# Kernel optimization log

Measured on AMD Instinct MI355X. Metric: run time of the kernel, lower is better.

## Reference

```python
import jax, jax.numpy as jnp
import numpy as np

N_HEAD = 8
LN_EPS = 1e-5


def layernorm(x, g, b):
    m = x.mean(-1, keepdims=True)
    var = x.var(-1, keepdims=True)
    return (x - m) / jnp.sqrt(var + LN_EPS) * g + b


def mha(xq, xkv, key_pad, w, b, wo, bo):
    # w: [3, D, D] (q,k,v proj), key_pad: [B, Nk] bool, True = ignore
    B, Nq, D = xq.shape
    H, dh = N_HEAD, D // N_HEAD
    q = (xq @ w[0] + b[0]).reshape(B, Nq, H, dh)
    k = (xkv @ w[1] + b[1]).reshape(B, -1, H, dh)
    v = (xkv @ w[2] + b[2]).reshape(B, -1, H, dh)
    s = jnp.einsum('bqhd,bkhd->bhqk', q, k) * (1.0 / np.float32(np.sqrt(dh)))
    s = jnp.where(key_pad[:, None, None, :], jnp.float32(-1e9), s)
    a = jax.nn.softmax(s, axis=-1)
    o = jnp.einsum('bhqk,bkhd->bqhd', a, v).reshape(B, Nq, D)
    return o @ wo + bo


def coattn_layer(v, q, v_pad, q_pad, aw, ab, awo, abo, lg, lb, fw1, fb1, fw2, fb2):
    # self-attention + residual + LN
    v_a = layernorm(v + mha(v, v, v_pad, aw[0], ab[0], awo[0], abo[0]), lg[0], lb[0])
    q_a = layernorm(q + mha(q, q, q_pad, aw[1], ab[1], awo[1], abo[1]), lg[1], lb[1])
    # cross attention: note qv_attn consumes OUTPUT of vq_attn (as in original)
    vq_out = mha(v_a, q_a, q_pad, aw[2], ab[2], awo[2], abo[2])
    qv_out = mha(q_a, vq_out, v_pad, aw[3], ab[3], awo[3], abo[3])
    v = layernorm(v + vq_out, lg[2], lb[2])
    q = layernorm(q + qv_out, lg[3], lb[3])
    # FFN (fc -> relu -> fc), residual + LN
    v = layernorm(v + (jax.nn.relu(v @ fw1[0] + fb1[0]) @ fw2[0] + fb2[0]), lg[4], lb[4])
    q = layernorm(q + (jax.nn.relu(q @ fw1[1] + fb1[1]) @ fw2[1] + fb2[1]), lg[5], lb[5])
    return v, q


def setup_inputs() -> dict:
    key = jax.random.key(0)
    B, NV, NQ, D, L = 8, 512, 512, 512, 4
    DF = 4 * D
    ks = jax.random.split(key, 12)
    sd = 0.02
    inp = {}
    inp['v'] = jax.random.normal(ks[0], (B, NV, D), jnp.float32)
    inp['q'] = jax.random.normal(ks[1], (B, NQ, D), jnp.float32)
    vm = jax.random.randint(ks[2], (B, NV), 0, 2, jnp.int32)
    qm = jax.random.randint(ks[3], (B, NQ), 0, 2, jnp.int32)
    inp['v_mask'] = vm.at[:, 0].set(1)  # ensure >=1 valid token per row
    inp['q_mask'] = qm.at[:, 0].set(1)
    inp['attn_w'] = sd * jax.random.normal(ks[4], (L, 4, 3, D, D), jnp.float32)
    inp['attn_b'] = jnp.zeros((L, 4, 3, D), jnp.float32)
    inp['attn_wo'] = sd * jax.random.normal(ks[5], (L, 4, D, D), jnp.float32)
    inp['attn_bo'] = jnp.zeros((L, 4, D), jnp.float32)
    inp['ln_g'] = jnp.ones((L, 6, D), jnp.float32)
    inp['ln_b'] = jnp.zeros((L, 6, D), jnp.float32)
    inp['ffn_w1'] = sd * jax.random.normal(ks[6], (L, 2, D, DF), jnp.float32)
    inp['ffn_b1'] = jnp.zeros((L, 2, DF), jnp.float32)
    inp['ffn_w2'] = sd * jax.random.normal(ks[7], (L, 2, DF, D), jnp.float32)
    inp['ffn_b2'] = jnp.zeros((L, 2, D), jnp.float32)
    inp['att_w'] = sd * jax.random.normal(ks[8], (D,), jnp.float32)
    inp['att_b'] = jnp.zeros((), jnp.float32)
    return inp


def reference(v, q, attn_w, attn_b, attn_wo, attn_bo, ln_g, ln_b,
              ffn_w1, ffn_b1, ffn_w2, ffn_b2, att_w, att_b, v_mask, q_mask):
    v_pad = v_mask == 0  # True = pad (original: ~v_mask.bool())
    q_pad = q_mask == 0
    L = attn_w.shape[0]
    for i in range(L):
        v, q = coattn_layer(v, q, v_pad, q_pad,
                            attn_w[i], attn_b[i], attn_wo[i], attn_bo[i],
                            ln_g[i], ln_b[i],
                            ffn_w1[i], ffn_b1[i], ffn_w2[i], ffn_b2[i])
    # att_net(v_i * q_j) is a bilinear form: sum_k v_bvk * q_bqk * w_k + bias
    s = jnp.einsum('bvk,bqk,k->bvq', v, q, att_w) + att_b
    cross_mask = v_pad[:, :, None] | q_pad[:, None, :]
    s = jnp.where(cross_mask, jnp.float32(-1e9), s)
    att_maps = jax.nn.softmax(s, axis=-1)
    v_num, q_num = v.shape[1], q.shape[1]
    seq_scale = 1.0 / np.float32(np.sqrt(v_num * q_num))
    return jnp.einsum('bvk,bvq,bqk->bk', v, att_maps, q) * seq_scale
```

## Files before the change

kernel.cpp:

```cpp
#include <hip/hip_runtime.h>
#include <hip/hip_bf16.h>

typedef __hip_bfloat16 bf16;
typedef __attribute__((ext_vector_type(8))) short short8;
typedef __attribute__((ext_vector_type(4))) short short4v;
typedef __attribute__((ext_vector_type(4))) float f32x4;

#define AS1 __attribute__((address_space(1)))
#define AS3 __attribute__((address_space(3)))

#define B_  8
#define N_  512
#define D_  512
#define H_  8
#define DH_ 64
#define DF_ 2048
#define L_  4

static __device__ __forceinline__ short bfbits(float x) {
  bf16 t = __float2bfloat16(x);
  return *reinterpret_cast<short*>(&t);
}

__global__ __launch_bounds__(256) void k_prep(const float* __restrict__ in,
                                              float* __restrict__ f,
                                              bf16* __restrict__ b, int n) {
  int i = blockIdx.x * 256 + threadIdx.x;
  if (i < n) { float v = in[i]; f[i] = v; b[i] = __float2bfloat16(v); }
}

__global__ __launch_bounds__(256) void k_wt(const float* __restrict__ aw_l,
                                            const float* __restrict__ awo_l,
                                            const float* __restrict__ fw1_l,
                                            const float* __restrict__ fw2_l,
                                            bf16* __restrict__ WT)
{
  __shared__ float Ls[32][33];
  int bx = blockIdx.x;
  const float* src; bf16* dst; int R, C, tr, tc;
  if (bx < 4096) {
    int id = bx >> 8, t = bx & 255;
    int m = id >> 2, part = id & 3;
    src = (part < 3) ? (aw_l + ((long)m * 3 + part) * D_ * D_)
                     : (awo_l + (long)m * D_ * D_);
    dst = WT + (long)id * 262144; R = 512; C = 512; tr = t >> 4; tc = t & 15;
  } else if (bx < 6144) {
    int q = bx - 4096; int id = q >> 10; int t = q & 1023;
    src = fw1_l + (long)id * D_ * DF_; dst = WT + 4194304 + (long)id * 1048576;
    R = 512; C = 2048; tr = t >> 6; tc = t & 63;
  } else {
    int q = bx - 6144; int id = q >> 10; int t = q & 1023;
    src = fw2_l + (long)id * DF_ * D_; dst = WT + 6291456 + (long)id * 1048576;
    R = 2048; C = 512; tr = t >> 4; tc = t & 15;
  }
  int tt = threadIdx.x;
#pragma unroll
  for (int p = 0; p < 4; ++p) {
    int idx = tt + p * 256; int lr = idx >> 5, lc = idx & 31;
    Ls[lr][lc] = src[(long)(tr * 32 + lr) * C + tc * 32 + lc];
  }
  __syncthreads();
#pragma unroll
  for (int p = 0; p < 4; ++p) {
    int idx = tt + p * 256; int lr = idx >> 5, lc = idx & 31;
    dst[(long)(tc * 32 + lr) * R + tr * 32 + lc] = __float2bfloat16(Ls[lc][lr]);
  }
}

template<int BN>
__global__ __launch_bounds__(256, 2) void k_mfma(
    const bf16* __restrict__ A, const bf16* __restrict__ A2,
    long aS, long aB, long aH, int lda,
    const bf16* __restrict__ Bm, long bS, long bB, long bH, int ldb,
    const float* __restrict__ bias, long biasS, float scale, int relu,
    float* __restrict__ Cf, long cfS, long cfB, long cfH, int ldcf,
    bf16* __restrict__ Cb, long cbS, long cbB, long cbH, int ldcb,
    int K, int Hh, int zPerS, int mode)
{
  constexpr int MI = (BN == 128) ? 4 : 2;
  constexpr int NI = 4;
  __shared__ short As[128 * 32];
  __shared__ short Bs[BN * 32];
  int tid = threadIdx.x;
  int w = tid >> 6, lane = tid & 63;
  int z = blockIdx.z;
  int s = z / zPerS; int zz = z - s * zPerS;
  int zb = zz / Hh, zh = zz - zb * Hh;
  int row0 = blockIdx.y * 128;
  int col0 = blockIdx.x * BN;
  const bf16* Asel = (mode == 1 && col0 >= 512) ? A2 : A;
  const bf16* Ab = Asel + s * aS + zb * aB + zh * aH;
  const bf16* Bb = Bm + s * bS + zb * bB + zh * bH;
  int rw = (BN == 128) ? ((w >> 1) * 64) : (w * 32);
  int cw = (BN == 128) ? ((w & 1) * 64) : 0;
  int quad = lane >> 4, l16 = lane & 15;

  f32x4 acc[MI][NI];
#pragma unroll
  for (int i = 0; i < MI; ++i)
#pragma unroll
    for (int j = 0; j < NI; ++j) acc[i][j] = {0.f, 0.f, 0.f, 0.f};

  for (int k0 = 0; k0 < K; k0 += 32) {
#pragma unroll
    for (int i = 0; i < 2; ++i) {
      int o = i * 4096 + w * 1024 + lane * 16;
      int r = o >> 6;
      const bf16* g = Ab + (long)(row0 + r) * lda + k0 + ((o & 63) >> 1);
      char* lp = (char*)As + i * 4096 + w * 1024;
      __builtin_amdgcn_global_load_lds((const AS1 void*)g, (AS3 void*)lp, 16, 0, 0);
    }
    constexpr int BI = (BN == 128) ? 2 : 1;
#pragma unroll
    for (int i = 0; i < BI; ++i) {
      int o = i * 4096 + w * 1024 + lane * 16;
      int r = o >> 6;
      const bf16* g = Bb + (long)(col0 + r) * ldb + k0 + ((o & 63) >> 1);
      char* lp = (char*)Bs + i * 4096 + w * 1024;
      __builtin_amdgcn_global_load_lds((const AS1 void*)g, (AS3 void*)lp, 16, 0, 0);
    }
    __syncthreads();
    short8 af[MI], bfr[NI];
#pragma unroll
    for (int mi = 0; mi < MI; ++mi)
      af[mi] = *(const short8*)&As[(rw + mi * 16 + l16) * 32 + quad * 8];
#pragma unroll
    for (int ni = 0; ni < NI; ++ni)
      bfr[ni] = *(const short8*)&Bs[(cw + ni * 16 + l16) * 32 + quad * 8];
#pragma unroll
    for (int mi = 0; mi < MI; ++mi)
#pragma unroll
      for (int ni = 0; ni < NI; ++ni)
        acc[mi][ni] = __builtin_amdgcn_mfma_f32_16x16x32_bf16(af[mi], bfr[ni], acc[mi][ni], 0, 0, 0);
    __syncthreads();
  }

  const float* bp = bias ? bias + s * biasS : nullptr;
#pragma unroll
  for (int mi = 0; mi < MI; ++mi)
#pragma unroll
    for (int ni = 0; ni < NI; ++ni) {
      int cg = col0 + cw + ni * 16 + l16;
      float bv = bp ? bp[cg] : 0.0f;
#pragma unroll
      for (int r = 0; r < 4; ++r) {
        int rg = row0 + rw + mi * 16 + quad * 4 + r;
        float v = acc[mi][ni][r] * scale + bv;
        if (relu) v = fmaxf(v, 0.0f);
        if (mode == 1) {
          bf16* base = Cb + s * cbS;
          if (cg < 512) base[(long)rg * 512 + cg] = __float2bfloat16(v);
          else if (cg < 1024) base[2097152 + (long)rg * 512 + (cg - 512)] = __float2bfloat16(v);
          else {
            int c2 = cg - 1024;
            base[4194304 + ((long)((rg >> 9) * 8 + (c2 >> 6)) * 64 + (c2 & 63)) * 512 + (rg & 511)]
                = __float2bfloat16(v);
          }
        } else {
          if (Cf) Cf[s * cfS + zb * cfB + zh * cfH + (long)rg * ldcf + cg] = v;
          if (Cb) Cb[s * cbS + zb * cbB + zh * cbH + (long)rg * ldcb + cg] = __float2bfloat16(v);
        }
      }
    }
}

__global__ __launch_bounds__(256, 2) void k_flash(
    const bf16* __restrict__ QKV, long sStride,
    const int* __restrict__ km0, const int* __restrict__ km1, float scale)
{
  __shared__ short Ks[2 * 128 * 32];
  __shared__ short Vs[4 * 64 * 32];
  __shared__ short Ps[4 * 64 * 32];
  int tid = threadIdx.x, w = tid >> 6, lane = tid & 63;
  int quad = lane >> 4, l16 = lane & 15;
  int s = blockIdx.z;
  const bf16* base = QKV + s * sStride;
  int bh = blockIdx.y, b = bh >> 3, h = bh & 7;
  int qt = blockIdx.x;
  const int* km = (s ? km1 : km0) + (b << 9);
  const bf16* Kg = base + 2097152;
  const bf16* Vt = base + 4194304;
  bf16* Og = (bf16*)base;

  int qrow = (b << 9) + (qt << 6) + (w << 4) + l16;
  short8 qf[2];
  qf[0] = *(const short8*)&base[(long)qrow * 512 + h * 64 + quad * 8];
  qf[1] = *(const short8*)&base[(long)qrow * 512 + h * 64 + 32 + quad * 8];

  float m_[4], l_[4];
  f32x4 acc_o[4];
#pragma unroll
  for (int r = 0; r < 4; ++r) { m_[r] = -3e38f; l_[r] = 0.f; }
#pragma unroll
  for (int ni = 0; ni < 4; ++ni) acc_o[ni] = {0.f, 0.f, 0.f, 0.f};

  for (int kt = 0; kt < 4; ++kt) {
    __syncthreads();
#pragma unroll
    for (int i = 0; i < 4; ++i) {
      int o = i * 4096 + w * 1024 + lane * 16;
      int kc = o >> 13, rem = o & 8191;
      int n = rem >> 6, cb = rem & 63;
      const bf16* g = Kg + ((long)((b << 9) + kt * 128 + n) << 9) + h * 64 + kc * 32 + (cb >> 1);
      char* lp = (char*)Ks + i * 4096 + w * 1024;
      __builtin_amdgcn_global_load_lds((const AS1 void*)g, (AS3 void*)lp, 16, 0, 0);
    }
#pragma unroll
    for (int i = 0; i < 4; ++i) {
      int o = i * 4096 + w * 1024 + lane * 16;
      int kc = o >> 12, rem = o & 4095;
      int d = rem >> 6, cb = rem & 63;
      const bf16* g = Vt + ((long)((bh << 6) + d) << 9) + kt * 128 + kc * 32 + (cb >> 1);
      char* lp = (char*)Vs + i * 4096 + w * 1024;
      __builtin_amdgcn_global_load_lds((const AS1 void*)g, (AS3 void*)lp, 16, 0, 0);
    }
    __syncthreads();
    f32x4 sa[8];
#pragma unroll
    for (int ni = 0; ni < 8; ++ni) sa[ni] = {0.f, 0.f, 0.f, 0.f};
#pragma unroll
    for (int kc = 0; kc < 2; ++kc)
#pragma unroll
      for (int ni = 0; ni < 8; ++ni) {
        short8 bfrag = *(const short8*)&Ks[kc * 4096 + (ni * 16 + l16) * 32 + quad * 8];
        sa[ni] = __builtin_amdgcn_mfma_f32_16x16x32_bf16(qf[kc], bfrag, sa[ni], 0, 0, 0);
      }
    float sv[8][4];
#pragma unroll
    for (int ni = 0; ni < 8; ++ni) {
      int kmv = km[kt * 128 + ni * 16 + l16];
#pragma unroll
      for (int r = 0; r < 4; ++r)
        sv[ni][r] = kmv ? sa[ni][r] * scale : -1e9f;
    }
#pragma unroll
    for (int r = 0; r < 4; ++r) {
      float rmax = sv[0][r];
#pragma unroll
      for (int ni = 1; ni < 8; ++ni) rmax = fmaxf(rmax, sv[ni][r]);
#pragma unroll
      for (int o = 1; o < 16; o <<= 1) rmax = fmaxf(rmax, __shfl_xor(rmax, o, 64));
      float newm = fmaxf(m_[r], rmax);
      float alpha = __expf(m_[r] - newm);
      float psum = 0.f;
#pragma unroll
      for (int ni = 0; ni < 8; ++ni) {
        float p = __expf(sv[ni][r] - newm);
        sv[ni][r] = p; psum += p;
      }
#pragma unroll
      for (int o = 1; o < 16; o <<= 1) psum += __shfl_xor(psum, o, 64);
      l_[r] = l_[r] * alpha + psum;
      m_[r] = newm;
#pragma unroll
      for (int ni = 0; ni < 4; ++ni) acc_o[ni][r] *= alpha;
    }
#pragma unroll
    for (int ni = 0; ni < 8; ++ni) {
      int j = ni * 16 + l16;
      short* pp = &Ps[(j >> 5) * 2048 + (w * 16 + quad * 4) * 32 + (j & 31)];
#pragma unroll
      for (int r = 0; r < 4; ++r) pp[r * 32] = bfbits(sv[ni][r]);
    }
    __syncthreads();
#pragma unroll
    for (int kcp = 0; kcp < 4; ++kcp) {
      short8 af = *(const short8*)&Ps[kcp * 2048 + (w * 16 + l16) * 32 + quad * 8];
#pragma unroll
      for (int ni = 0; ni < 4; ++ni) {
        short8 bfrag = *(const short8*)&Vs[kcp * 2048 + (ni * 16 + l16) * 32 + quad * 8];
        acc_o[ni] = __builtin_amdgcn_mfma_f32_16x16x32_bf16(af, bfrag, acc_o[ni], 0, 0, 0);
      }
    }
  }
  float linv[4];
#pragma unroll
  for (int r = 0; r < 4; ++r) linv[r] = 1.0f / l_[r];
#pragma unroll
  for (int ni = 0; ni < 4; ++ni)
#pragma unroll
    for (int r = 0; r < 4; ++r) {
      long row = (b << 9) + (qt << 6) + (w << 4) + quad * 4 + r;
      Og[row * 512 + h * 64 + ni * 16 + l16] = __float2bfloat16(acc_o[ni][r] * linv[r]);
    }
}

__global__ __launch_bounds__(256) void k_ln2(
    const float* x0, const float* r0, const float* g0, const float* b0,
    float* yf0, bf16* yb0,
    const float* x1, const float* r1, const float* g1, const float* b1,
    float* yf1, bf16* yb1)
{
  int sel = blockIdx.x >> 12;
  long row = blockIdx.x & 4095;
  const float* x = sel ? x1 : x0;
  const float* r = sel ? r1 : r0;
  const float* g = sel ? g1 : g0;
  const float* bb = sel ? b1 : b0;
  float* yf = sel ? yf1 : yf0;
  bf16* yb = sel ? yb1 : yb0;
  int t = threadIdx.x;
  const float* xr = x + row * D_;
  const float* rr = r + row * D_;
  float v0 = xr[t] + rr[t];
  float v1 = xr[t + 256] + rr[t + 256];
  float s = v0 + v1;
  float ss = v0 * v0 + v1 * v1;
#pragma unroll
  for (int o = 32; o > 0; o >>= 1) {
    s += __shfl_down(s, o, 64);
    ss += __shfl_down(ss, o, 64);
  }
  __shared__ float rs[4];
  __shared__ float rss[4];
  int lane = t & 63, wid = t >> 6;
  if (lane == 0) { rs[wid] = s; rss[wid] = ss; }
  __syncthreads();
  s = rs[0] + rs[1] + rs[2] + rs[3];
  ss = rss[0] + rss[1] + rss[2] + rss[3];
  float mean = s * (1.0f / D_);
  float var = ss * (1.0f / D_) - mean * mean;
  float rstd = rsqrtf(var + 1e-5f);
  float o0 = (v0 - mean) * rstd * g[t]       + bb[t];
  float o1 = (v1 - mean) * rstd * g[t + 256] + bb[t + 256];
  if (yf) { float* yr = yf + row * D_; yr[t] = o0; yr[t + 256] = o1; }
  if (yb) { bf16* yr = yb + row * D_; yr[t] = __float2bfloat16(o0); yr[t + 256] = __float2bfloat16(o1); }
}

__global__ __launch_bounds__(256) void k_softmax_x(float* __restrict__ S,
                                                   const int* __restrict__ vm,
                                                   const int* __restrict__ qm)
{
  int wrow = blockIdx.x * 4 + (threadIdx.x >> 6);
  int lane = threadIdx.x & 63;
  int b = wrow >> 9, i = wrow & 511;
  bool rowpad = (vm[(b << 9) + i] == 0);
  float* p = S + (long)wrow * 512;
  const int* qb = qm + (b << 9);
  int j0 = lane * 8;
  float4 a0 = *(const float4*)(p + j0);
  float4 a1 = *(const float4*)(p + j0 + 4);
  int4 m0 = *(const int4*)(qb + j0);
  int4 m1 = *(const int4*)(qb + j0 + 4);
  float v[8];
  v[0] = (rowpad || !m0.x) ? -1e9f : a0.x; v[1] = (rowpad || !m0.y) ? -1e9f : a0.y;
  v[2] = (rowpad || !m0.z) ? -1e9f : a0.z; v[3] = (rowpad || !m0.w) ? -1e9f : a0.w;
  v[4] = (rowpad || !m1.x) ? -1e9f : a1.x; v[5] = (rowpad || !m1.y) ? -1e9f : a1.y;
  v[6] = (rowpad || !m1.z) ? -1e9f : a1.z; v[7] = (rowpad || !m1.w) ? -1e9f : a1.w;
  float mx = v[0];
#pragma unroll
  for (int u = 1; u < 8; ++u) mx = fmaxf(mx, v[u]);
#pragma unroll
  for (int o = 1; o < 64; o <<= 1) mx = fmaxf(mx, __shfl_xor(mx, o, 64));
  float e[8], sum = 0.f;
#pragma unroll
  for (int u = 0; u < 8; ++u) { e[u] = __expf(v[u] - mx); sum += e[u]; }
#pragma unroll
  for (int o = 1; o < 64; o <<= 1) sum += __shfl_xor(sum, o, 64);
  float inv = 1.0f / sum;
  bf16 ob[8];
#pragma unroll
  for (int u = 0; u < 8; ++u) ob[u] = __float2bfloat16(e[u] * inv);
  bf16* pb = (bf16*)p;
  *(short8*)&pb[j0] = *(const short8*)ob;
}

__global__ __launch_bounds__(256) void k_vwqt(const float* __restrict__ V,
                                              const float* __restrict__ Q,
                                              const float* __restrict__ w,
                                              bf16* __restrict__ Vw, bf16* __restrict__ Qt)
{
  __shared__ float Ls[32][33];
  int bx = blockIdx.x, t = threadIdx.x;
  if (bx < 2048) {
    int i = bx * 1024 + t * 4;
    float4 v = *(const float4*)(V + i);
    int k = i & 511;
    bf16 o[4] = { __float2bfloat16(v.x * w[k]),     __float2bfloat16(v.y * w[k + 1]),
                  __float2bfloat16(v.z * w[k + 2]), __float2bfloat16(v.w * w[k + 3]) };
    *(short4v*)&Vw[i] = *(const short4v*)o;
  } else {
    int q = bx - 2048; int b = q >> 8; int tq = q & 255;
    int tr = tq >> 4, tc = tq & 15;
    const float* Qb = Q + (long)b * 262144;
    bf16* Qtb = Qt + (long)b * 262144;
#pragma unroll
    for (int p = 0; p < 4; ++p) {
      int idx = t + p * 256; int lr = idx >> 5, lc = idx & 31;
      Ls[lr][lc] = Qb[(long)(tr * 32 + lr) * 512 + tc * 32 + lc];
    }
    __syncthreads();
#pragma unroll
    for (int p = 0; p < 4; ++p) {
      int idx = t + p * 256; int lr = idx >> 5, lc = idx & 31;
      Qtb[(long)(tc * 32 + lr) * 512 + tr * 32 + lc] = __float2bfloat16(Ls[lc][lr]);
    }
  }
}

__global__ __launch_bounds__(256) void k_final_out(
    const float* __restrict__ V, const float* __restrict__ QT, float* __restrict__ out)
{
  int b = blockIdx.x >> 1;
  int k = ((blockIdx.x & 1) << 8) + threadIdx.x;
  const float* Vb = V + (long)b * N_ * D_ + k;
  const float* Tb = QT + (long)b * N_ * D_ + k;
  float acc = 0.0f;
  for (int i = 0; i < N_; ++i) acc += Vb[(long)i * D_] * Tb[(long)i * D_];
  out[b * D_ + k] = acc * (1.0f / 512.0f);
}

extern "C" void kernel_launch(void* const* d_in, const int* in_sizes, int n_in,
                              void* d_out, int out_size, void* d_ws, size_t ws_size,
                              hipStream_t stream)
{
  const float* in_v   = (const float*)d_in[0];
  const float* in_q   = (const float*)d_in[1];
  const int*   v_mask = (const int*)  d_in[2];
  const int*   q_mask = (const int*)  d_in[3];
  const float* aw  = (const float*)d_in[4];
  const float* ab  = (const float*)d_in[5];
  const float* awo = (const float*)d_in[6];
  const float* abo = (const float*)d_in[7];
  const float* lg  = (const float*)d_in[8];
  const float* lb  = (const float*)d_in[9];
  const float* fw1 = (const float*)d_in[10];
  const float* fb1 = (const float*)d_in[11];
  const float* fw2 = (const float*)d_in[12];
  const float* fb2 = (const float*)d_in[13];
  const float* atw = (const float*)d_in[14];
  const float* atb = (const float*)d_in[15];
  float* out = (float*)d_out;
  (void)atb;

  const int SZ = B_ * N_ * D_;
  char* wsb = (char*)d_ws;
  const long MB = 1024L * 1024;
  float* Vcur   = (float*)(wsb + 0 * MB);
  float* Qcur   = (float*)(wsb + 8 * MB);
  float* T      = (float*)(wsb + 16 * MB);
  bf16*  WT     = (bf16*) (wsb + 24 * MB);
  bf16*  Vcur_b = (bf16*) (wsb + 40 * MB);
  bf16*  Qcur_b = (bf16*) (wsb + 44 * MB);
  bf16*  VA_b   = (bf16*) (wsb + 48 * MB);
  bf16*  QA_b   = (bf16*) (wsb + 52 * MB);
  bf16*  VQ_b   = (bf16*) (wsb + 56 * MB);
  bf16*  QKV0   = (bf16*) (wsb + 60 * MB);
  bf16*  Hid    = (bf16*) (wsb + 84 * MB);
  float* T2     = (float*)(wsb + 116 * MB);
  float* Sf     = (float*)(wsb + 124 * MB);
  bf16*  Vw_b   = (bf16*) (wsb + 132 * MB);
  bf16*  Qt_b   = (bf16*) (wsb + 136 * MB);

  const long ZBIG = 1000000;
  const long TSTR = (long)(T2 - T);

  k_prep<<<8192, 256, 0, stream>>>(in_v, Vcur, Vcur_b, SZ);
  k_prep<<<8192, 256, 0, stream>>>(in_q, Qcur, Qcur_b, SZ);

  for (int l = 0; l < L_; ++l) {
    const float* lgl = lg + (long)l * 6 * D_;
    const float* lbl = lb + (long)l * 6 * D_;
    k_wt<<<8192, 256, 0, stream>>>(aw + (long)l * 12 * 262144,
                                   awo + (long)l * 4 * 262144,
                                   fw1 + (long)l * 2 * 1048576,
                                   fw2 + (long)l * 2 * 1048576, WT);
    k_mfma<128><<<dim3(12, 32, 2), 256, 0, stream>>>(
        Vcur_b, Vcur_b, 2097152, 0, 0, 512,
        WT, 1048576, 0, 0, 512,
        ab + (long)l * 4 * 1536, 1536, 1.f, 0,
        nullptr, 0, 0, 0, 0, QKV0, 6291456, 0, 0, 0,
        512, 1, 1, 1);
    k_flash<<<dim3(8, 64, 2), 256, 0, stream>>>(QKV0, 6291456, v_mask, q_mask, 0.125f);
    k_mfma<128><<<dim3(4, 32, 2), 256, 0, stream>>>(
        QKV0, QKV0, 6291456, 0, 0, 512,
        WT + 3 * 262144, 1048576, 0, 0, 512,
        abo + (long)l * 4 * 512, 512, 1.f, 0,
        T, TSTR, 0, 0, 512, nullptr, 0, 0, 0, 0,
        512, 1, 1, 0);
    k_ln2<<<8192, 256, 0, stream>>>(Vcur, T,  lgl + 0 * D_, lbl + 0 * D_, nullptr, VA_b,
                                    Qcur, T2, lgl + 1 * D_, lbl + 1 * D_, nullptr, QA_b);
    k_mfma<128><<<dim3(12, 32, 1), 256, 0, stream>>>(
        VA_b, QA_b, 0, 0, 0, 512,
        WT + 2 * 1048576, 0, 0, 0, 512,
        ab + (long)(l * 4 + 2) * 1536, 0, 1.f, 0,
        nullptr, 0, 0, 0, 0, QKV0, 0, 0, 0, 0,
        512, 1, 1, 1);
    k_flash<<<dim3(8, 64, 1), 256, 0, stream>>>(QKV0, 0, q_mask, q_mask, 0.125f);
    k_mfma<128><<<dim3(4, 32, 1), 256, 0, stream>>>(
        QKV0, QKV0, 0, 0, 0, 512,
        WT + (2 * 4 + 3) * 262144, 0, 0, 0, 512,
        abo + (long)(l * 4 + 2) * 512, 0, 1.f, 0,
        T, 0, 0, 0, 512, VQ_b, 0, 0, 0, 512,
        512, 1, 1, 0);
    k_mfma<128><<<dim3(12, 32, 1), 256, 0, stream>>>(
        QA_b, VQ_b, 0, 0, 0, 512,
        WT + 3 * 1048576, 0, 0, 0, 512,
        ab + (long)(l * 4 + 3) * 1536, 0, 1.f, 0,
        nullptr, 0, 0, 0, 0, QKV0, 0, 0, 0, 0,
        512, 1, 1, 1);
    k_flash<<<dim3(8, 64, 1), 256, 0, stream>>>(QKV0, 0, v_mask, v_mask, 0.125f);
    k_mfma<128><<<dim3(4, 32, 1), 256, 0, stream>>>(
        QKV0, QKV0, 0, 0, 0, 512,
        WT + (3 * 4 + 3) * 262144, 0, 0, 0, 512,
        abo + (long)(l * 4 + 3) * 512, 0, 1.f, 0,
        T2, 0, 0, 0, 512, nullptr, 0, 0, 0, 0,
        512, 1, 1, 0);
    k_ln2<<<8192, 256, 0, stream>>>(Vcur, T,  lgl + 2 * D_, lbl + 2 * D_, Vcur, Vcur_b,
                                    Qcur, T2, lgl + 3 * D_, lbl + 3 * D_, Qcur, Qcur_b);
    k_mfma<128><<<dim3(16, 32, 2), 256, 0, stream>>>(
        Vcur_b, Vcur_b, 2097152, 0, 0, 512,
        WT + 4194304, 1048576, 0, 0, 512,
        fb1 + (long)l * 2 * 2048, 2048, 1.f, 1,
        nullptr, 0, 0, 0, 0, Hid, 8388608, 0, 0, 2048,
        512, 1, 1, 0);
    k_mfma<128><<<dim3(4, 32, 2), 256, 0, stream>>>(
        Hid, Hid, 8388608, 0, 0, 2048,
        WT + 6291456, 1048576, 0, 0, 2048,
        fb2 + (long)l * 2 * 512, 512, 1.f, 0,
        T, TSTR, 0, 0, 512, nullptr, 0, 0, 0, 0,
        2048, 1, 1, 0);
    k_ln2<<<8192, 256, 0, stream>>>(Vcur, T,  lgl + 4 * D_, lbl + 4 * D_, Vcur, Vcur_b,
                                    Qcur, T2, lgl + 5 * D_, lbl + 5 * D_, Qcur, Qcur_b);
  }

  k_vwqt<<<4096, 256, 0, stream>>>(Vcur, Qcur, atw, Vw_b, Qt_b);
  k_mfma<128><<<dim3(4, 4, 8), 256, 0, stream>>>(
      Vw_b, Vw_b, 0, 262144, 0, 512, Qcur_b, 0, 262144, 0, 512,
      nullptr, 0, 1.f, 0,
      Sf, 0, 262144, 0, 512, nullptr, 0, 0, 0, 0,
      512, 1, ZBIG, 0);
  k_softmax_x<<<1024, 256, 0, stream>>>(Sf, v_mask, q_mask);
  k_mfma<128><<<dim3(4, 4, 8), 256, 0, stream>>>(
      (const bf16*)Sf, (const bf16*)Sf, 0, 524288, 0, 1024, Qt_b, 0, 262144, 0, 512,
      nullptr, 0, 1.f, 0,
      T, 0, 262144, 0, 512, nullptr, 0, 0, 0, 0,
      512, 1, ZBIG, 0);
  k_final_out<<<16, 256, 0, stream>>>(Vcur, T, out);

  (void)in_sizes; (void)n_in; (void)out_size; (void)ws_size;
}
```

Baseline: 1.571 ms.

## Split-K the N=512 output projections and fuse partial-sum reduction into LayerNorm

The output-projection and FFN-down GEMMs (N=512, only 128-256 blocks) now split K into two halves via an extra grid z dimension, each writing fp32 partials to separate buffers. The LayerNorm kernel sums both partials with the residual, replacing the old single-result add. The cross-attention projections also switch to the 64-wide tile, and a small kernel sums partials into bf16 for VQ. The aim is more blocks to fill the GPU, at the cost of extra fp32 partial traffic and one more launch.

```diff
diff --git a/kernel.cpp b/kernel.cpp
--- a/kernel.cpp
+++ b/kernel.cpp
@@ -75,7 +75,7 @@
     const float* __restrict__ bias, long biasS, float scale, int relu,
     float* __restrict__ Cf, long cfS, long cfB, long cfH, int ldcf,
     bf16* __restrict__ Cb, long cbS, long cbB, long cbH, int ldcb,
-    int K, int Hh, int zPerS, int mode)
+    int kLen, int Hh, int zPerS, int mode, int kSplit, long pStride)
 {
   constexpr int MI = (BN == 128) ? 4 : 2;
   constexpr int NI = 4;
@@ -84,13 +84,15 @@
   int tid = threadIdx.x;
   int w = tid >> 6, lane = tid & 63;
   int z = blockIdx.z;
+  int kk = 0;
+  if (kSplit > 1) { kk = z % kSplit; z /= kSplit; }
   int s = z / zPerS; int zz = z - s * zPerS;
   int zb = zz / Hh, zh = zz - zb * Hh;
   int row0 = blockIdx.y * 128;
   int col0 = blockIdx.x * BN;
   const bf16* Asel = (mode == 1 && col0 >= 512) ? A2 : A;
-  const bf16* Ab = Asel + s * aS + zb * aB + zh * aH;
-  const bf16* Bb = Bm + s * bS + zb * bB + zh * bH;
+  const bf16* Ab = Asel + s * aS + zb * aB + zh * aH + (long)kk * kLen;
+  const bf16* Bb = Bm + s * bS + zb * bB + zh * bH + (long)kk * kLen;
   int rw = (BN == 128) ? ((w >> 1) * 64) : (w * 32);
   int cw = (BN == 128) ? ((w & 1) * 64) : 0;
   int quad = lane >> 4, l16 = lane & 15;
@@ -101,7 +103,7 @@
 #pragma unroll
     for (int j = 0; j < NI; ++j) acc[i][j] = {0.f, 0.f, 0.f, 0.f};
 
-  for (int k0 = 0; k0 < K; k0 += 32) {
+  for (int k0 = 0; k0 < kLen; k0 += 32) {
 #pragma unroll
     for (int i = 0; i < 2; ++i) {
       int o = i * 4096 + w * 1024 + lane * 16;
@@ -135,7 +137,7 @@
     __syncthreads();
   }
 
-  const float* bp = bias ? bias + s * biasS : nullptr;
+  const float* bp = (bias && kk == 0) ? bias + s * biasS : nullptr;
 #pragma unroll
   for (int mi = 0; mi < MI; ++mi)
 #pragma unroll
@@ -157,7 +159,7 @@
                 = __float2bfloat16(v);
           }
         } else {
-          if (Cf) Cf[s * cfS + zb * cfB + zh * cfH + (long)rg * ldcf + cg] = v;
+          if (Cf) Cf[s * cfS + (long)kk * pStride + zb * cfB + zh * cfH + (long)rg * ldcf + cg] = v;
           if (Cb) Cb[s * cbS + zb * cbB + zh * cbH + (long)rg * ldcb + cg] = __float2bfloat16(v);
         }
       }
@@ -286,24 +288,23 @@
 }
 
 __global__ __launch_bounds__(256) void k_ln2(
-    const float* x0, const float* r0, const float* g0, const float* b0,
-    float* yf0, bf16* yb0,
-    const float* x1, const float* r1, const float* g1, const float* b1,
-    float* yf1, bf16* yb1)
+    const float* x0, const float* g0, const float* b0, float* yf0, bf16* yb0,
+    const float* x1, const float* g1, const float* b1, float* yf1, bf16* yb1,
+    const float* __restrict__ P, long pstr)
 {
   int sel = blockIdx.x >> 12;
   long row = blockIdx.x & 4095;
   const float* x = sel ? x1 : x0;
-  const float* r = sel ? r1 : r0;
   const float* g = sel ? g1 : g0;
   const float* bb = sel ? b1 : b0;
   float* yf = sel ? yf1 : yf0;
   bf16* yb = sel ? yb1 : yb0;
   int t = threadIdx.x;
   const float* xr = x + row * D_;
-  const float* rr = r + row * D_;
-  float v0 = xr[t] + rr[t];
-  float v1 = xr[t + 256] + rr[t + 256];
+  const float* ra = P + (sel ? 2 : 0) * pstr + row * D_;
+  const float* rb = ra + pstr;
+  float v0 = xr[t] + ra[t] + rb[t];
+  float v1 = xr[t + 256] + ra[t + 256] + rb[t + 256];
   float s = v0 + v1;
   float ss = v0 * v0 + v1 * v1;
 #pragma unroll
@@ -325,6 +326,18 @@
   float o1 = (v1 - mean) * rstd * g[t + 256] + bb[t + 256];
   if (yf) { float* yr = yf + row * D_; yr[t] = o0; yr[t + 256] = o1; }
   if (yb) { bf16* yr = yb + row * D_; yr[t] = __float2bfloat16(o0); yr[t + 256] = __float2bfloat16(o1); }
+}
+
+__global__ __launch_bounds__(256) void k_sum2bf(const float* __restrict__ a,
+                                                const float* __restrict__ b,
+                                                bf16* __restrict__ o)
+{
+  int i = (blockIdx.x * 256 + threadIdx.x) * 4;
+  float4 va = *(const float4*)(a + i);
+  float4 vb = *(const float4*)(b + i);
+  bf16 ov[4] = { __float2bfloat16(va.x + vb.x), __float2bfloat16(va.y + vb.y),
+                 __float2bfloat16(va.z + vb.z), __float2bfloat16(va.w + vb.w) };
+  *(short4v*)&o[i] = *(const short4v*)ov;
 }
 
 __global__ __launch_bounds__(256) void k_softmax_x(float* __restrict__ S,
@@ -438,22 +451,22 @@
   const long MB = 1024L * 1024;
   float* Vcur   = (float*)(wsb + 0 * MB);
   float* Qcur   = (float*)(wsb + 8 * MB);
-  float* T      = (float*)(wsb + 16 * MB);
-  bf16*  WT     = (bf16*) (wsb + 24 * MB);
-  bf16*  Vcur_b = (bf16*) (wsb + 40 * MB);
-  bf16*  Qcur_b = (bf16*) (wsb + 44 * MB);
-  bf16*  VA_b   = (bf16*) (wsb + 48 * MB);
-  bf16*  QA_b   = (bf16*) (wsb + 52 * MB);
-  bf16*  VQ_b   = (bf16*) (wsb + 56 * MB);
-  bf16*  QKV0   = (bf16*) (wsb + 60 * MB);
-  bf16*  Hid    = (bf16*) (wsb + 84 * MB);
-  float* T2     = (float*)(wsb + 116 * MB);
-  float* Sf     = (float*)(wsb + 124 * MB);
-  bf16*  Vw_b   = (bf16*) (wsb + 132 * MB);
-  bf16*  Qt_b   = (bf16*) (wsb + 136 * MB);
+  float* P0     = (float*)(wsb + 16 * MB);
+  const long PSZ = 2097152;
+  bf16*  WT     = (bf16*) (wsb + 48 * MB);
+  bf16*  Vcur_b = (bf16*) (wsb + 64 * MB);
+  bf16*  Qcur_b = (bf16*) (wsb + 68 * MB);
+  bf16*  VA_b   = (bf16*) (wsb + 72 * MB);
+  bf16*  QA_b   = (bf16*) (wsb + 76 * MB);
+  bf16*  VQ_b   = (bf16*) (wsb + 80 * MB);
+  bf16*  QKV0   = (bf16*) (wsb + 84 * MB);
+  bf16*  Hid    = (bf16*) (wsb + 108 * MB);
+  float* Sf     = P0;
+  bf16*  Vw_b   = (bf16*) (wsb + 24 * MB);
+  bf16*  Qt_b   = (bf16*) (wsb + 28 * MB);
+  float* Tfin   = (float*)(wsb + 32 * MB);
 
   const long ZBIG = 1000000;
-  const long TSTR = (long)(T2 - T);
 
   k_prep<<<8192, 256, 0, stream>>>(in_v, Vcur, Vcur_b, SZ);
   k_prep<<<8192, 256, 0, stream>>>(in_q, Qcur, Qcur_b, SZ);
@@ -470,58 +483,62 @@
         WT, 1048576, 0, 0, 512,
         ab + (long)l * 4 * 1536, 1536, 1.f, 0,
         nullptr, 0, 0, 0, 0, QKV0, 6291456, 0, 0, 0,
-        512, 1, 1, 1);
+        512, 1, 1, 1, 1, 0);
     k_flash<<<dim3(8, 64, 2), 256, 0, stream>>>(QKV0, 6291456, v_mask, q_mask, 0.125f);
-    k_mfma<128><<<dim3(4, 32, 2), 256, 0, stream>>>(
+    k_mfma<128><<<dim3(4, 32, 4), 256, 0, stream>>>(
         QKV0, QKV0, 6291456, 0, 0, 512,
         WT + 3 * 262144, 1048576, 0, 0, 512,
         abo + (long)l * 4 * 512, 512, 1.f, 0,
-        T, TSTR, 0, 0, 512, nullptr, 0, 0, 0, 0,
-        512, 1, 1, 0);
-    k_ln2<<<8192, 256, 0, stream>>>(Vcur, T,  lgl + 0 * D_, lbl + 0 * D_, nullptr, VA_b,
-                                    Qcur, T2, lgl + 1 * D_, lbl + 1 * D_, nullptr, QA_b);
+        P0, 2 * PSZ, 0, 0, 512, nullptr, 0, 0, 0, 0,
+        256, 1, 1, 0, 2, PSZ);
+    k_ln2<<<8192, 256, 0, stream>>>(Vcur, lgl + 0 * D_, lbl + 0 * D_, nullptr, VA_b,
+                                    Qcur, lgl + 1 * D_, lbl + 1 * D_, nullptr, QA_b,
+                                    P0, PSZ);
     k_mfma<128><<<dim3(12, 32, 1), 256, 0, stream>>>(
         VA_b, QA_b, 0, 0, 0, 512,
         WT + 2 * 1048576, 0, 0, 0, 512,
         ab + (long)(l * 4 + 2) * 1536, 0, 1.f, 0,
         nullptr, 0, 0, 0, 0, QKV0, 0, 0, 0, 0,
-        512, 1, 1, 1);
+        512, 1, 1, 1, 1, 0);
     k_flash<<<dim3(8, 64, 1), 256, 0, stream>>>(QKV0, 0, q_mask, q_mask, 0.125f);
-    k_mfma<128><<<dim3(4, 32, 1), 256, 0, stream>>>(
+    k_mfma<64><<<dim3(8, 32, 2), 256, 0, stream>>>(
         QKV0, QKV0, 0, 0, 0, 512,
         WT + (2 * 4 + 3) * 262144, 0, 0, 0, 512,
         abo + (long)(l * 4 + 2) * 512, 0, 1.f, 0,
-        T, 0, 0, 0, 512, VQ_b, 0, 0, 0, 512,
-        512, 1, 1, 0);
+        P0, 0, 0, 0, 512, nullptr, 0, 0, 0, 0,
+        256, 1, 1, 0, 2, PSZ);
+    k_sum2bf<<<2048, 256, 0, stream>>>(P0, P0 + PSZ, VQ_b);
     k_mfma<128><<<dim3(12, 32, 1), 256, 0, stream>>>(
         QA_b, VQ_b, 0, 0, 0, 512,
         WT + 3 * 1048576, 0, 0, 0, 512,
         ab + (long)(l * 4 + 3) * 1536, 0, 1.f, 0,
         nullptr, 0, 0, 0, 0, QKV0, 0, 0, 0, 0,
-        512, 1, 1, 1);
+        512, 1, 1, 1, 1, 0);
     k_flash<<<dim3(8, 64, 1), 256, 0, stream>>>(QKV0, 0, v_mask, v_mask, 0.125f);
-    k_mfma<128><<<dim3(4, 32, 1), 256, 0, stream>>>(
+    k_mfma<64><<<dim3(8, 32, 2), 256, 0, stream>>>(
         QKV0, QKV0, 0, 0, 0, 512,
         WT + (3 * 4 + 3) * 262144, 0, 0, 0, 512,
         abo + (long)(l * 4 + 3) * 512, 0, 1.f, 0,
-        T2, 0, 0, 0, 512, nullptr, 0, 0, 0, 0,
-        512, 1, 1, 0);
-    k_ln2<<<8192, 256, 0, stream>>>(Vcur, T,  lgl + 2 * D_, lbl + 2 * D_, Vcur, Vcur_b,
-                                    Qcur, T2, lgl + 3 * D_, lbl + 3 * D_, Qcur, Qcur_b);
+        P0 + 2 * PSZ, 0, 0, 0, 512, nullptr, 0, 0, 0, 0,
+        256, 1, 1, 0, 2, PSZ);
+    k_ln2<<<8192, 256, 0, stream>>>(Vcur, lgl + 2 * D_, lbl + 2 * D_, Vcur, Vcur_b,
+                                    Qcur, lgl + 3 * D_, lbl + 3 * D_, Qcur, Qcur_b,
+                                    P0, PSZ);
     k_mfma<128><<<dim3(16, 32, 2), 256, 0, stream>>>(
         Vcur_b, Vcur_b, 2097152, 0, 0, 512,
         WT + 4194304, 1048576, 0, 0, 512,
         fb1 + (long)l * 2 * 2048, 2048, 1.f, 1,
         nullptr, 0, 0, 0, 0, Hid, 8388608, 0, 0, 2048,
-        512, 1, 1, 0);
-    k_mfma<128><<<dim3(4, 32, 2), 256, 0, stream>>>(
+        512, 1, 1, 0, 1, 0);
+    k_mfma<128><<<dim3(4, 32, 4), 256, 0, stream>>>(
         Hid, Hid, 8388608, 0, 0, 2048,
         WT + 6291456, 1048576, 0, 0, 2048,
         fb2 + (long)l * 2 * 512, 512, 1.f, 0,
-        T, TSTR, 0, 0, 512, nullptr, 0, 0, 0, 0,
-        2048, 1, 1, 0);
-    k_ln2<<<8192, 256, 0, stream>>>(Vcur, T,  lgl + 4 * D_, lbl + 4 * D_, Vcur, Vcur_b,
-                                    Qcur, T2, lgl + 5 * D_, lbl + 5 * D_, Qcur, Qcur_b);
+        P0, 2 * PSZ, 0, 0, 512, nullptr, 0, 0, 0, 0,
+        1024, 1, 1, 0, 2, PSZ);
+    k_ln2<<<8192, 256, 0, stream>>>(Vcur, lgl + 4 * D_, lbl + 4 * D_, Vcur, Vcur_b,
+                                    Qcur, lgl + 5 * D_, lbl + 5 * D_, Qcur, Qcur_b,
+                                    P0, PSZ);
   }
 
   k_vwqt<<<4096, 256, 0, stream>>>(Vcur, Qcur, atw, Vw_b, Qt_b);
@@ -529,14 +546,14 @@
       Vw_b, Vw_b, 0, 262144, 0, 512, Qcur_b, 0, 262144, 0, 512,
       nullptr, 0, 1.f, 0,
       Sf, 0, 262144, 0, 512, nullptr, 0, 0, 0, 0,
-      512, 1, ZBIG, 0);
+      512, 1, ZBIG, 0, 1, 0);
   k_softmax_x<<<1024, 256, 0, stream>>>(Sf, v_mask, q_mask);
   k_mfma<128><<<dim3(4, 4, 8), 256, 0, stream>>>(
       (const bf16*)Sf, (const bf16*)Sf, 0, 524288, 0, 1024, Qt_b, 0, 262144, 0, 512,
       nullptr, 0, 1.f, 0,
-      T, 0, 262144, 0, 512, nullptr, 0, 0, 0, 0,
-      512, 1, ZBIG, 0);
-  k_final_out<<<16, 256, 0, stream>>>(Vcur, T, out);
+      Tfin, 0, 262144, 0, 512, nullptr, 0, 0, 0, 0,
+      512, 1, ZBIG, 0, 1, 0);
+  k_final_out<<<16, 256, 0, stream>>>(Vcur, Tfin, out);
 
   (void)in_sizes; (void)n_in; (void)out_size; (void)ws_size;
 }
```

After: 1.507 ms. 1.04x faster.
